# Kernel tuning notes

Measured on AMD Instinct MI355X. Metric: run time of the kernel, lower is better.

The kernel has to match this reference:

```python
import jax, jax.numpy as jnp
import numpy as np

NUM_HEADS = 8
NUM_Q = 64
RANK = 64
DIM = 768
LN_EPS = 1e-5


def setup_inputs() -> dict:
    key = jax.random.key(0)
    ks = jax.random.split(key, 8)
    b, n = 4, 1024
    x = jax.random.normal(ks[0], (b, NUM_Q, DIM), dtype=jnp.float32)
    context = jax.random.normal(ks[1], (b, n, DIM), dtype=jnp.float32)
    s = 0.02
    Wq = jax.random.normal(ks[2], (DIM, DIM), dtype=jnp.float32) * s
    Wk = jax.random.normal(ks[3], (DIM, DIM), dtype=jnp.float32) * s
    Wv1 = jax.random.normal(ks[4], (DIM, NUM_Q * RANK), dtype=jnp.float32) * s
    ln_g = jnp.ones((NUM_Q * RANK,), dtype=jnp.float32)
    ln_b = jnp.zeros((NUM_Q * RANK,), dtype=jnp.float32)
    Wc = jax.random.normal(ks[5], (NUM_Q, RANK, DIM), dtype=jnp.float32) * s
    Wout = jax.random.normal(ks[6], (DIM, DIM), dtype=jnp.float32) * s
    return {"x": x, "context": context, "Wq": Wq, "Wk": Wk, "Wv1": Wv1,
            "ln_g": ln_g, "ln_b": ln_b, "Wc": Wc, "Wout": Wout}


def reference(x, context, Wq, Wk, Wv1, ln_g, ln_b, Wc, Wout):
    b, nq, d = x.shape
    n = context.shape[1]
    h, dh = NUM_HEADS, d // NUM_HEADS

    q = x @ Wq                      # [b, nq, d]
    k = context @ Wk                # [b, n, d]

    # q-aware V: Linear -> LayerNorm(all_q_mid) -> grouped 1x1 conv (per-query rank->d)
    h1 = context @ Wv1              # [b, n, NUM_Q*RANK]
    mu = jnp.mean(h1, axis=-1, keepdims=True)
    var = jnp.var(h1, axis=-1, keepdims=True)
    h1 = (h1 - mu) * jax.lax.rsqrt(var + LN_EPS) * ln_g + ln_b
    vmid = h1.reshape(b, n, NUM_Q, RANK)
    v = jnp.einsum('bnqr,qrd->bqnd', vmid, Wc)   # [b, NUM_Q, n, d]
    # split heads: 'b q n (h dh) -> b h q n dh'
    v = v.reshape(b, NUM_Q, n, h, dh).transpose(0, 3, 1, 2, 4)

    qh = q.reshape(b, nq, h, dh).transpose(0, 2, 1, 3)   # [b,h,nq,dh]
    kh = k.reshape(b, n, h, dh).transpose(0, 2, 1, 3)    # [b,h,n,dh]
    scale = dh ** (-0.25)
    sim = jnp.einsum('bhid,bhjd->bhij', qh * scale, kh * scale)
    attn = jax.nn.softmax(sim, axis=-1)                  # [b,h,nq,n]
    out = jnp.einsum('bhij,bhijd->bhid', attn, v)        # per-query V
    out = out.transpose(0, 2, 1, 3).reshape(b, nq, d)
    return out @ Wout
```

## Files before the change

kernel.cpp:

```cpp
#include <hip/hip_runtime.h>
#include <math.h>

typedef unsigned short ushort_t;
typedef __bf16 bf16x8 __attribute__((ext_vector_type(8)));
typedef float f32x4 __attribute__((ext_vector_type(4)));

__device__ __forceinline__ ushort_t f2b_rne(float f) {
    union { float f; unsigned int u; } c;
    c.f = f;
    unsigned int u = c.u;
    u += 0x7FFFu + ((u >> 16) & 1u);
    return (ushort_t)(u >> 16);
}
__device__ __forceinline__ float b2f(ushort_t v) {
    union { unsigned int u; float f; } c;
    c.u = ((unsigned int)v) << 16;
    return c.f;
}

__device__ __forceinline__ void gl_lds16(const ushort_t* g, ushort_t* l) {
    __builtin_amdgcn_global_load_lds(
        (const __attribute__((address_space(1))) void*)g,
        (__attribute__((address_space(3))) void*)l, 16, 0, 0);
}

__global__ __launch_bounds__(256) void prep(
    const float* __restrict__ x, const float* __restrict__ context,
    const float* __restrict__ Wq, const float* __restrict__ Wk,
    const float* __restrict__ Wv1, const float* __restrict__ Wout,
    ushort_t* __restrict__ x_b, ushort_t* __restrict__ ctx_b,
    ushort_t* __restrict__ Wq_t, ushort_t* __restrict__ Wk_t,
    ushort_t* __restrict__ Wv1_t, ushort_t* __restrict__ Wout_t,
    int b, int n) {
    const int t = threadIdx.x;
    const int bid = blockIdx.x;
    const int nb_x = (b * 64 * 768 / 4) / 256;
    const int nb_c = (b * n * 768 / 4) / 256;

    if (bid < nb_x + nb_c) {
        const float* in = (bid < nb_x) ? x : context;
        ushort_t* outp = (bid < nb_x) ? x_b : ctx_b;
        const int i = ((bid < nb_x) ? bid : (bid - nb_x)) * 256 + t;
        float4 v = ((const float4*)in)[i];
        ushort_t o[4] = {f2b_rne(v.x), f2b_rne(v.y), f2b_rne(v.z), f2b_rne(v.w)};
        *(uint2*)&outp[(size_t)i * 4] = *(uint2*)o;
        return;
    }

    int u = bid - nb_x - nb_c;
    const float* in;
    ushort_t* outp;
    int R = 768, C = 768;
    if (u < 576)        { in = Wq;  outp = Wq_t; }
    else if (u < 1152)  { u -= 576;  in = Wk;  outp = Wk_t; }
    else if (u < 4224)  { u -= 1152; in = Wv1; outp = Wv1_t; C = 4096; }
    else                { u -= 4224; in = Wout; outp = Wout_t; }
    const int ct = C / 32;
    const int c0 = (u % ct) * 32, r0 = (u / ct) * 32;
    const int tx = t & 31, ty = t >> 5;

    __shared__ float tt[32][33];
#pragma unroll
    for (int i = 0; i < 4; i++)
        tt[ty + 8 * i][tx] = in[(size_t)(r0 + ty + 8 * i) * C + c0 + tx];
    __syncthreads();
#pragma unroll
    for (int i = 0; i < 4; i++)
        outp[(size_t)(c0 + ty + 8 * i) * R + r0 + tx] = f2b_rne(tt[tx][ty + 8 * i]);
}

__global__ __launch_bounds__(256) void gemm3(
    const ushort_t* __restrict__ x_b, const ushort_t* __restrict__ ctx_b,
    const ushort_t* __restrict__ Wq_t, const ushort_t* __restrict__ Wk_t,
    const ushort_t* __restrict__ Wv1_t,
    ushort_t* __restrict__ qb, ushort_t* __restrict__ kb,
    ushort_t* __restrict__ h1b, int b, int n) {
    const int bid = blockIdx.x;
    const int tq = (b * 64 / 128) * 6;
    const int tk = (b * n / 128) * 6;

    const ushort_t *A, *Bt;
    ushort_t* C;
    int N, row0, col0;
    if (bid < tq) {
        A = x_b; Bt = Wq_t; C = qb; N = 768;
        row0 = (bid / 6) * 128; col0 = (bid % 6) * 128;
    } else if (bid < tq + tk) {
        const int u = bid - tq;
        A = ctx_b; Bt = Wk_t; C = kb; N = 768;
        row0 = (u / 6) * 128; col0 = (u % 6) * 128;
    } else {
        const int u = bid - tq - tk;
        A = ctx_b; Bt = Wv1_t; C = h1b; N = 4096;
        row0 = (u / 32) * 128; col0 = (u % 32) * 128;
    }
    const int K = 768;

    __shared__ ushort_t As[128 * 32];
    __shared__ ushort_t Bs[128 * 32];

    const int t = threadIdx.x;
    const int lane = t & 63;
    const int wave = t >> 6;
    const int quad = lane >> 4;
    const int l15 = lane & 15;
    const int wm = (wave >> 1) * 64;
    const int wn = (wave & 1) * 64;

    const ushort_t* ga0 = A + (size_t)(row0 + (t >> 2)) * K + (t & 3) * 8;
    const ushort_t* ga1 = ga0 + (size_t)64 * K;
    const ushort_t* gb0 = Bt + (size_t)(col0 + (t >> 2)) * K + (t & 3) * 8;
    const ushort_t* gb1 = gb0 + (size_t)64 * K;

    ushort_t* lA0 = &As[wave * 512];
    ushort_t* lA1 = &As[2048 + wave * 512];
    ushort_t* lB0 = &Bs[wave * 512];
    ushort_t* lB1 = &Bs[2048 + wave * 512];

    f32x4 acc[4][4] = {};

    for (int k0 = 0; k0 < K; k0 += 32) {
        __syncthreads();
        gl_lds16(ga0 + k0, lA0);
        gl_lds16(ga1 + k0, lA1);
        gl_lds16(gb0 + k0, lB0);
        gl_lds16(gb1 + k0, lB1);
        __syncthreads();

        bf16x8 af[4], bfr[4];
#pragma unroll
        for (int i = 0; i < 4; i++)
            af[i] = *(const bf16x8*)&As[(wm + i * 16 + l15) * 32 + quad * 8];
#pragma unroll
        for (int j = 0; j < 4; j++)
            bfr[j] = *(const bf16x8*)&Bs[(wn + j * 16 + l15) * 32 + quad * 8];
#pragma unroll
        for (int i = 0; i < 4; i++)
#pragma unroll
            for (int j = 0; j < 4; j++)
                acc[i][j] = __builtin_amdgcn_mfma_f32_16x16x32_bf16(
                    af[i], bfr[j], acc[i][j], 0, 0, 0);
    }

#pragma unroll
    for (int i = 0; i < 4; i++)
#pragma unroll
        for (int j = 0; j < 4; j++)
#pragma unroll
            for (int r = 0; r < 4; r++) {
                const int row = row0 + wm + i * 16 + quad * 4 + r;
                const int col = col0 + wn + j * 16 + l15;
                C[(size_t)row * N + col] = f2b_rne(acc[i][j][r]);
            }
}

__global__ __launch_bounds__(256) void stats_scores(
    const ushort_t* __restrict__ h1b, const ushort_t* __restrict__ qb,
    const ushort_t* __restrict__ kb, float* __restrict__ mu,
    float* __restrict__ rstd, float* __restrict__ S, int b, int n) {
    __shared__ ushort_t sb[192 * 104];
    const int bid = blockIdx.x;
    const int t = threadIdx.x;

    if (bid < b * n) {
        float* red = (float*)sb;
        const ushort_t* p = h1b + (size_t)bid * 4096;
        float v[16];
#pragma unroll
        for (int g = 0; g < 2; g++) {
            bf16x8 xv = *(const bf16x8*)&p[(t + g * 256) * 8];
#pragma unroll
            for (int j = 0; j < 8; j++) v[g * 8 + j] = (float)xv[j];
        }
        float s = 0.f;
#pragma unroll
        for (int i = 0; i < 16; i++) s += v[i];
        red[t] = s;
        __syncthreads();
        for (int off = 128; off > 0; off >>= 1) {
            if (t < off) red[t] += red[t + off];
            __syncthreads();
        }
        const float m = red[0] * (1.0f / 4096.0f);
        __syncthreads();
        float s2 = 0.f;
#pragma unroll
        for (int i = 0; i < 16; i++) { const float d = v[i] - m; s2 += d * d; }
        red[t] = s2;
        __syncthreads();
        for (int off = 128; off > 0; off >>= 1) {
            if (t < off) red[t] += red[t + off];
            __syncthreads();
        }
        if (t == 0) {
            mu[bid] = m;
            rstd[bid] = rsqrtf(red[0] * (1.0f / 4096.0f) + 1e-5f);
        }
        return;
    }

    const int sid = bid - b * n;
    const int nt = n / 128;
    const int n0 = (sid % nt) * 128;
    const int bh = sid / nt;
    const int bb = bh >> 3, h = bh & 7;
    const int lane = t & 63, wave = t >> 6;
    const int quad = lane >> 4, l15 = lane & 15;
    const int wm = (wave >> 1) * 32;
    const int wn = (wave & 1) * 64;

    ushort_t* Qs = sb;
    ushort_t* Ks = sb + 64 * 104;

    for (int g = t; g < 768; g += 256) {
        const int r = g / 12, s = g - r * 12;
        *(bf16x8*)&Qs[r * 104 + s * 8] =
            *(const bf16x8*)&qb[(size_t)(bb * 64 + r) * 768 + h * 96 + s * 8];
    }
    for (int g = t; g < 1536; g += 256) {
        const int r = g / 12, s = g - r * 12;
        *(bf16x8*)&Ks[r * 104 + s * 8] =
            *(const bf16x8*)&kb[(size_t)(bb * n + n0 + r) * 768 + h * 96 + s * 8];
    }
    __syncthreads();

    f32x4 acc[2][4] = {};
#pragma unroll
    for (int ks = 0; ks < 3; ks++) {
        bf16x8 af[2], bfr[4];
#pragma unroll
        for (int i = 0; i < 2; i++)
            af[i] = *(const bf16x8*)&Qs[(wm + i * 16 + l15) * 104 + ks * 32 + quad * 8];
#pragma unroll
        for (int j = 0; j < 4; j++)
            bfr[j] = *(const bf16x8*)&Ks[(wn + j * 16 + l15) * 104 + ks * 32 + quad * 8];
#pragma unroll
        for (int i = 0; i < 2; i++)
#pragma unroll
            for (int j = 0; j < 4; j++)
                acc[i][j] = __builtin_amdgcn_mfma_f32_16x16x32_bf16(
                    af[i], bfr[j], acc[i][j], 0, 0, 0);
    }

    const float sc = 0.10206207261596575f;
    float* Sp = S + (size_t)bh * 64 * n;
#pragma unroll
    for (int i = 0; i < 2; i++)
#pragma unroll
        for (int j = 0; j < 4; j++)
#pragma unroll
            for (int r = 0; r < 4; r++) {
                const int row = wm + i * 16 + quad * 4 + r;
                const int col = n0 + wn + j * 16 + l15;
                Sp[(size_t)row * n + col] = acc[i][j][r] * sc;
            }
}

__global__ __launch_bounds__(256) void attn_pv(
    const float* __restrict__ S, const float* __restrict__ mu,
    const float* __restrict__ rstd, const ushort_t* __restrict__ h1b,
    float* __restrict__ Apart, int n, int nsp) {
    const int sp = blockIdx.x;
    const int bq = blockIdx.y;
    const int bb = bq >> 6, qi = bq & 63;
    const int k0 = sp * 128;
    const int tid = threadIdx.x;
    const int lane = tid & 63, w = tid >> 6;
    const int k = tid & 127, hg = tid >> 7;

    __shared__ float sS[2048];
    __shared__ float smu[128], srs[128];
    __shared__ float cw[16];
    __shared__ float sm[8], sl[8], swmu[8];

    const size_t Sbase = ((size_t)(bb * 512) + qi) * n + k0;
    for (int i = tid; i < 1024; i += 256) {
        const int h = i >> 7, kk = i & 127;
        sS[i] = S[Sbase + (size_t)h * 64 * n + kk];
    }
    if (tid < 128) {
        smu[tid] = mu[(size_t)bb * n + k0 + tid];
        srs[tid] = rstd[(size_t)bb * n + k0 + tid];
    }
    __syncthreads();

    float r4[4];
#pragma unroll
    for (int hh = 0; hh < 4; hh++) r4[hh] = sS[(hg * 4 + hh) * 128 + k];
#pragma unroll
    for (int off = 32; off > 0; off >>= 1)
#pragma unroll
        for (int hh = 0; hh < 4; hh++) r4[hh] = fmaxf(r4[hh], __shfl_down(r4[hh], off));
    if (lane == 0)
#pragma unroll
        for (int hh = 0; hh < 4; hh++) cw[w * 4 + hh] = r4[hh];
    __syncthreads();
    if (tid < 8) {
        const int g2 = tid >> 2, hh = tid & 3;
        sm[tid] = fmaxf(cw[(2 * g2) * 4 + hh], cw[(2 * g2 + 1) * 4 + hh]);
    }
    __syncthreads();

    float wm4[4];
#pragma unroll
    for (int hh = 0; hh < 4; hh++) {
        const int h = hg * 4 + hh;
        const float e = expf(sS[h * 128 + k] - sm[h]);
        const float wv = e * srs[k];
        sS[h * 128 + k] = wv;
        r4[hh] = e;
        wm4[hh] = wv * smu[k];
    }
#pragma unroll
    for (int off = 32; off > 0; off >>= 1)
#pragma unroll
        for (int hh = 0; hh < 4; hh++) r4[hh] += __shfl_down(r4[hh], off);
    if (lane == 0)
#pragma unroll
        for (int hh = 0; hh < 4; hh++) cw[w * 4 + hh] = r4[hh];
    __syncthreads();
    if (tid < 8) {
        const int g2 = tid >> 2, hh = tid & 3;
        sl[tid] = cw[(2 * g2) * 4 + hh] + cw[(2 * g2 + 1) * 4 + hh];
    }
    __syncthreads();
#pragma unroll
    for (int off = 32; off > 0; off >>= 1)
#pragma unroll
        for (int hh = 0; hh < 4; hh++) wm4[hh] += __shfl_down(wm4[hh], off);
    if (lane == 0)
#pragma unroll
        for (int hh = 0; hh < 4; hh++) cw[w * 4 + hh] = wm4[hh];
    __syncthreads();
    if (tid < 8) {
        const int g2 = tid >> 2, hh = tid & 3;
        swmu[tid] = cw[(2 * g2) * 4 + hh] + cw[(2 * g2 + 1) * 4 + hh];
    }

    const ushort_t* vp =
        h1b + ((size_t)bb * n + k0 + w * 32) * 4096 + qi * 64 + lane;
    float acc[8] = {};
    for (int o = 0; o < 32; o += 8) {
        float v[8];
#pragma unroll
        for (int j = 0; j < 8; j++) v[j] = b2f(vp[(size_t)(o + j) * 4096]);
#pragma unroll
        for (int h = 0; h < 8; h++) {
            const float4 wa = *(const float4*)&sS[h * 128 + w * 32 + o];
            const float4 wb = *(const float4*)&sS[h * 128 + w * 32 + o + 4];
            acc[h] += wa.x * v[0] + wa.y * v[1] + wa.z * v[2] + wa.w * v[3] +
                      wb.x * v[4] + wb.y * v[5] + wb.z * v[6] + wb.w * v[7];
        }
    }
    __syncthreads();
#pragma unroll
    for (int h = 0; h < 8; h++) sS[w * 512 + h * 64 + lane] = acc[h];
    __syncthreads();

    float* Ap = Apart + ((size_t)bq * nsp + sp) * 544;
#pragma unroll
    for (int s = 0; s < 2; s++) {
        const int o = tid + s * 256;
        Ap[o] = sS[o] + sS[512 + o] + sS[1024 + o] + sS[1536 + o];
    }
    if (tid < 8) {
        Ap[512 + tid] = sm[tid];
        Ap[520 + tid] = sl[tid];
        Ap[528 + tid] = swmu[tid];
    }
}

__global__ __launch_bounds__(256) void merge_wc(
    const float* __restrict__ Apart, const float* __restrict__ ln_g,
    const float* __restrict__ ln_b, const float* __restrict__ Wc,
    ushort_t* __restrict__ outp, int nsp) {
    const int bq = blockIdx.x;
    const int qi = bq & 63;
    const int tid = threadIdx.x;

    __shared__ float sA[512];
    __shared__ float sst[8 * 24];

    for (int i = tid; i < nsp * 24; i += 256) {
        const int sp = i / 24, j = i - sp * 24;
        sst[sp * 24 + j] = Apart[((size_t)bq * nsp + sp) * 544 + 512 + j];
    }
    __syncthreads();

#pragma unroll
    for (int s = 0; s < 2; s++) {
        const int o = tid + s * 256;
        const int h = o >> 6, rr = o & 63;
        float m = -1e30f;
        for (int sp = 0; sp < nsp; sp++) m = fmaxf(m, sst[sp * 24 + h]);
        float l = 0.f, wm = 0.f, v = 0.f;
        for (int sp = 0; sp < nsp; sp++) {
            const float scl = expf(sst[sp * 24 + h] - m);
            l += scl * sst[sp * 24 + 8 + h];
            wm += scl * sst[sp * 24 + 16 + h];
            v += scl * Apart[((size_t)bq * nsp + sp) * 544 + o];
        }
        const int c = qi * 64 + rr;
        sA[o] = ln_g[c] * ((v - wm) / l) + ln_b[c];
    }
    __syncthreads();

    for (int d = tid; d < 768; d += 256) {
        const int h = d / 96;
        const float* wp = Wc + (size_t)qi * 49152 + d;
        float a = 0.f;
#pragma unroll
        for (int r = 0; r < 64; r++) a += sA[h * 64 + r] * wp[(size_t)r * 768];
        outp[(size_t)bq * 768 + d] = f2b_rne(a);
    }
}

__global__ __launch_bounds__(256) void gemm_out(const ushort_t* __restrict__ A,
                                                const ushort_t* __restrict__ Bt,
                                                float* __restrict__ C,
                                                int M, int N, int K) {
    __shared__ ushort_t As[128 * 40];
    __shared__ ushort_t Bs[128 * 40];

    const int t = threadIdx.x;
    const int lane = t & 63;
    const int wave = t >> 6;
    const int quad = lane >> 4;
    const int l15 = lane & 15;
    const int wm = (wave >> 1) * 64;
    const int wn = (wave & 1) * 64;
    const int row0 = blockIdx.y * 128, col0 = blockIdx.x * 128;

    const int srow = t >> 2;
    const int sseg = t & 3;
    const ushort_t* ga0 = A + (size_t)(row0 + srow) * K + sseg * 8;
    const ushort_t* ga1 = A + (size_t)(row0 + srow + 64) * K + sseg * 8;
    const ushort_t* gb0 = Bt + (size_t)(col0 + srow) * K + sseg * 8;
    const ushort_t* gb1 = Bt + (size_t)(col0 + srow + 64) * K + sseg * 8;

    f32x4 acc[4][4] = {};

    bf16x8 ra0 = *(const bf16x8*)ga0;
    bf16x8 ra1 = *(const bf16x8*)ga1;
    bf16x8 rb0 = *(const bf16x8*)gb0;
    bf16x8 rb1 = *(const bf16x8*)gb1;

    for (int k0 = 0; k0 < K; k0 += 32) {
        __syncthreads();
        *(bf16x8*)&As[srow * 40 + sseg * 8] = ra0;
        *(bf16x8*)&As[(srow + 64) * 40 + sseg * 8] = ra1;
        *(bf16x8*)&Bs[srow * 40 + sseg * 8] = rb0;
        *(bf16x8*)&Bs[(srow + 64) * 40 + sseg * 8] = rb1;
        __syncthreads();
        if (k0 + 32 < K) {
            ra0 = *(const bf16x8*)(ga0 + k0 + 32);
            ra1 = *(const bf16x8*)(ga1 + k0 + 32);
            rb0 = *(const bf16x8*)(gb0 + k0 + 32);
            rb1 = *(const bf16x8*)(gb1 + k0 + 32);
        }
        bf16x8 af[4], bfr[4];
#pragma unroll
        for (int i = 0; i < 4; i++)
            af[i] = *(const bf16x8*)&As[(wm + i * 16 + l15) * 40 + quad * 8];
#pragma unroll
        for (int j = 0; j < 4; j++)
            bfr[j] = *(const bf16x8*)&Bs[(wn + j * 16 + l15) * 40 + quad * 8];
#pragma unroll
        for (int i = 0; i < 4; i++)
#pragma unroll
            for (int j = 0; j < 4; j++)
                acc[i][j] = __builtin_amdgcn_mfma_f32_16x16x32_bf16(
                    af[i], bfr[j], acc[i][j], 0, 0, 0);
    }

#pragma unroll
    for (int i = 0; i < 4; i++)
#pragma unroll
        for (int j = 0; j < 4; j++)
#pragma unroll
            for (int r = 0; r < 4; r++) {
                const int row = row0 + wm + i * 16 + quad * 4 + r;
                const int col = col0 + wn + j * 16 + l15;
                C[(size_t)row * N + col] = acc[i][j][r];
            }
}

extern "C" void kernel_launch(void* const* d_in, const int* in_sizes, int n_in,
                              void* d_out, int out_size, void* d_ws, size_t ws_size,
                              hipStream_t stream) {
    const float* x       = (const float*)d_in[0];
    const float* context = (const float*)d_in[1];
    const float* Wq      = (const float*)d_in[2];
    const float* Wk      = (const float*)d_in[3];
    const float* Wv1     = (const float*)d_in[4];
    const float* ln_g    = (const float*)d_in[5];
    const float* ln_b    = (const float*)d_in[6];
    const float* Wc      = (const float*)d_in[7];
    const float* Wout    = (const float*)d_in[8];
    float* out = (float*)d_out;

    const int b = in_sizes[0] / (64 * 768);
    const int n = in_sizes[1] / (b * 768);
    const int M  = b * 64;
    const int Mn = b * n;
    const int nsp = n / 128;

    float* ws = (float*)d_ws;
    size_t off = 0;
    float* S     = ws + off;  off += (size_t)b * 8 * 64 * n;
    float* Apart = ws + off;  off += (size_t)M * nsp * 544;
    float* muh   = ws + off;  off += (size_t)Mn;
    float* rstdh = ws + off;  off += (size_t)Mn;

    ushort_t* us = (ushort_t*)(ws + off);
    size_t uo = 0;
    ushort_t* x_b    = us + uo;  uo += (size_t)M * 768;
    ushort_t* ctx_b  = us + uo;  uo += (size_t)Mn * 768;
    ushort_t* qb     = us + uo;  uo += (size_t)M * 768;
    ushort_t* kb     = us + uo;  uo += (size_t)Mn * 768;
    ushort_t* h1b    = us + uo;  uo += (size_t)Mn * 4096;
    ushort_t* Wq_t   = us + uo;  uo += (size_t)768 * 768;
    ushort_t* Wk_t   = us + uo;  uo += (size_t)768 * 768;
    ushort_t* Wv1_t  = us + uo;  uo += (size_t)4096 * 768;
    ushort_t* Wout_t = us + uo;  uo += (size_t)768 * 768;
    ushort_t* outp_b = us + uo;  uo += (size_t)M * 768;

    const int nb_x = (M * 768 / 4) / 256;
    const int nb_c = (Mn * 768 / 4) / 256;
    prep<<<nb_x + nb_c + 576 * 3 + 3072, 256, 0, stream>>>(
        x, context, Wq, Wk, Wv1, Wout, x_b, ctx_b, Wq_t, Wk_t, Wv1_t, Wout_t, b, n);

    const int tq = (M / 128) * 6, tk = (Mn / 128) * 6, th = (Mn / 128) * 32;
    gemm3<<<tq + tk + th, 256, 0, stream>>>(x_b, ctx_b, Wq_t, Wk_t, Wv1_t,
                                            qb, kb, h1b, b, n);

    stats_scores<<<Mn + b * 8 * (n / 128), 256, 0, stream>>>(
        h1b, qb, kb, muh, rstdh, S, b, n);

    attn_pv<<<dim3(nsp, M), 256, 0, stream>>>(S, muh, rstdh, h1b, Apart, n, nsp);

    merge_wc<<<M, 256, 0, stream>>>(Apart, ln_g, ln_b, Wc, outp_b, nsp);

    gemm_out<<<dim3(6, M / 128), 256, 0, stream>>>(outp_b, Wout_t, out, M, 768, 768);
}
```

Before: 203.1 us.

## Fuse LayerNorm stats into h1 GEMM epilogue and fuse attention with merge

The h1 projection is now computed transposed (Wv1 rows by context tokens), and its GEMM epilogue accumulates per-token sum and sum-of-squares via atomics. This removes the separate LayerNorm statistics pass over h1. Attention, PV and the Wc merge become one kernel per query that runs full-length softmax and does the PV product with MFMA over contiguous transposed h1 rows, dropping the split-K partials buffer and the merge kernel. In exchange, variance comes from E[x^2]-mean^2, which is less precise, the atomics add contention, and each attention block now handles all n keys serially with lower grid parallelism.

```diff
diff --git a/kernel.cpp b/kernel.cpp
--- a/kernel.cpp
+++ b/kernel.cpp
@@ -31,6 +31,7 @@
     ushort_t* __restrict__ x_b, ushort_t* __restrict__ ctx_b,
     ushort_t* __restrict__ Wq_t, ushort_t* __restrict__ Wk_t,
     ushort_t* __restrict__ Wv1_t, ushort_t* __restrict__ Wout_t,
+    float* __restrict__ colzero,
     int b, int n) {
     const int t = threadIdx.x;
     const int bid = blockIdx.x;
@@ -48,6 +49,12 @@
     }
 
     int u = bid - nb_x - nb_c;
+    if (u >= 4800) {
+        const int idx = (u - 4800) * 256 + t;
+        ((float4*)colzero)[idx] = make_float4(0.f, 0.f, 0.f, 0.f);
+        return;
+    }
+
     const float* in;
     ushort_t* outp;
     int R = 768, C = 768;
@@ -74,14 +81,17 @@
     const ushort_t* __restrict__ Wq_t, const ushort_t* __restrict__ Wk_t,
     const ushort_t* __restrict__ Wv1_t,
     ushort_t* __restrict__ qb, ushort_t* __restrict__ kb,
-    ushort_t* __restrict__ h1b, int b, int n) {
+    ushort_t* __restrict__ h1t, float* __restrict__ colsum,
+    float* __restrict__ colsumsq, int b, int n) {
     const int bid = blockIdx.x;
     const int tq = (b * 64 / 128) * 6;
     const int tk = (b * n / 128) * 6;
+    const int Mn = b * n;
 
     const ushort_t *A, *Bt;
     ushort_t* C;
     int N, row0, col0;
+    bool is_h1 = false;
     if (bid < tq) {
         A = x_b; Bt = Wq_t; C = qb; N = 768;
         row0 = (bid / 6) * 128; col0 = (bid % 6) * 128;
@@ -91,8 +101,10 @@
         row0 = (u / 6) * 128; col0 = (u % 6) * 128;
     } else {
         const int u = bid - tq - tk;
-        A = ctx_b; Bt = Wv1_t; C = h1b; N = 4096;
-        row0 = (u / 32) * 128; col0 = (u % 32) * 128;
+        A = Wv1_t; Bt = ctx_b; C = h1t; N = Mn;
+        const int ct = Mn / 128;
+        row0 = (u / ct) * 128; col0 = (u % ct) * 128;
+        is_h1 = true;
     }
     const int K = 768;
 
@@ -152,65 +164,45 @@
                 const int col = col0 + wn + j * 16 + l15;
                 C[(size_t)row * N + col] = f2b_rne(acc[i][j][r]);
             }
-}
-
-__global__ __launch_bounds__(256) void stats_scores(
-    const ushort_t* __restrict__ h1b, const ushort_t* __restrict__ qb,
-    const ushort_t* __restrict__ kb, float* __restrict__ mu,
-    float* __restrict__ rstd, float* __restrict__ S, int b, int n) {
-    __shared__ ushort_t sb[192 * 104];
-    const int bid = blockIdx.x;
+
+    if (is_h1) {
+#pragma unroll
+        for (int j = 0; j < 4; j++) {
+            float vs = 0.f, vq = 0.f;
+#pragma unroll
+            for (int i = 0; i < 4; i++)
+#pragma unroll
+                for (int r = 0; r < 4; r++) {
+                    const float v = acc[i][j][r];
+                    vs += v;
+                    vq += v * v;
+                }
+            vs += __shfl_xor(vs, 16); vs += __shfl_xor(vs, 32);
+            vq += __shfl_xor(vq, 16); vq += __shfl_xor(vq, 32);
+            if (quad == 0) {
+                const int col = col0 + wn + j * 16 + l15;
+                atomicAdd(&colsum[col], vs);
+                atomicAdd(&colsumsq[col], vq);
+            }
+        }
+    }
+}
+
+__global__ __launch_bounds__(256) void scores_mfma(const ushort_t* __restrict__ qb,
+                                                   const ushort_t* __restrict__ kb,
+                                                   float* __restrict__ S, int n) {
+    const int nt = n / 128;
+    const int n0 = (blockIdx.x % nt) * 128;
+    const int bh = blockIdx.x / nt;
+    const int bb = bh >> 3, h = bh & 7;
     const int t = threadIdx.x;
-
-    if (bid < b * n) {
-        float* red = (float*)sb;
-        const ushort_t* p = h1b + (size_t)bid * 4096;
-        float v[16];
-#pragma unroll
-        for (int g = 0; g < 2; g++) {
-            bf16x8 xv = *(const bf16x8*)&p[(t + g * 256) * 8];
-#pragma unroll
-            for (int j = 0; j < 8; j++) v[g * 8 + j] = (float)xv[j];
-        }
-        float s = 0.f;
-#pragma unroll
-        for (int i = 0; i < 16; i++) s += v[i];
-        red[t] = s;
-        __syncthreads();
-        for (int off = 128; off > 0; off >>= 1) {
-            if (t < off) red[t] += red[t + off];
-            __syncthreads();
-        }
-        const float m = red[0] * (1.0f / 4096.0f);
-        __syncthreads();
-        float s2 = 0.f;
-#pragma unroll
-        for (int i = 0; i < 16; i++) { const float d = v[i] - m; s2 += d * d; }
-        red[t] = s2;
-        __syncthreads();
-        for (int off = 128; off > 0; off >>= 1) {
-            if (t < off) red[t] += red[t + off];
-            __syncthreads();
-        }
-        if (t == 0) {
-            mu[bid] = m;
-            rstd[bid] = rsqrtf(red[0] * (1.0f / 4096.0f) + 1e-5f);
-        }
-        return;
-    }
-
-    const int sid = bid - b * n;
-    const int nt = n / 128;
-    const int n0 = (sid % nt) * 128;
-    const int bh = sid / nt;
-    const int bb = bh >> 3, h = bh & 7;
     const int lane = t & 63, wave = t >> 6;
     const int quad = lane >> 4, l15 = lane & 15;
     const int wm = (wave >> 1) * 32;
     const int wn = (wave & 1) * 64;
 
-    ushort_t* Qs = sb;
-    ushort_t* Ks = sb + 64 * 104;
+    __shared__ ushort_t Qs[64 * 104];
+    __shared__ ushort_t Ks[128 * 104];
 
     for (int g = t; g < 768; g += 256) {
         const int r = g / 12, s = g - r * 12;
@@ -256,152 +248,99 @@
             }
 }
 
-__global__ __launch_bounds__(256) void attn_pv(
-    const float* __restrict__ S, const float* __restrict__ mu,
-    const float* __restrict__ rstd, const ushort_t* __restrict__ h1b,
-    float* __restrict__ Apart, int n, int nsp) {
-    const int sp = blockIdx.x;
-    const int bq = blockIdx.y;
+__global__ __launch_bounds__(256) void attn_fused(
+    const float* __restrict__ S, const float* __restrict__ colsum,
+    const float* __restrict__ colsumsq, const ushort_t* __restrict__ h1t,
+    const float* __restrict__ ln_g, const float* __restrict__ ln_b,
+    const float* __restrict__ Wc, ushort_t* __restrict__ outp,
+    int n, int Mn) {
+    const int bq = blockIdx.x;
     const int bb = bq >> 6, qi = bq & 63;
-    const int k0 = sp * 128;
     const int tid = threadIdx.x;
-    const int lane = tid & 63, w = tid >> 6;
-    const int k = tid & 127, hg = tid >> 7;
-
-    __shared__ float sS[2048];
-    __shared__ float smu[128], srs[128];
-    __shared__ float cw[16];
+    const int lane = tid & 63, wv = tid >> 6;
+    const int quad = lane >> 4, l15 = lane & 15;
+
+    __shared__ ushort_t sW[9 * 1032];
+    __shared__ ushort_t sH[64 * 264];
     __shared__ float sm[8], sl[8], swmu[8];
-
-    const size_t Sbase = ((size_t)(bb * 512) + qi) * n + k0;
-    for (int i = tid; i < 1024; i += 256) {
-        const int h = i >> 7, kk = i & 127;
-        sS[i] = S[Sbase + (size_t)h * 64 * n + kk];
-    }
-    if (tid < 128) {
-        smu[tid] = mu[(size_t)bb * n + k0 + tid];
-        srs[tid] = rstd[(size_t)bb * n + k0 + tid];
-    }
+    __shared__ float sA[512];
+
+    float* sMu = (float*)sH;
+    float* sRs = (float*)sH + 1024;
+
+    for (int i = tid; i < n; i += 256) {
+        const float cs = colsum[bb * n + i];
+        const float cq = colsumsq[bb * n + i];
+        const float m = cs * (1.0f / 4096.0f);
+        sMu[i] = m;
+        sRs[i] = rsqrtf(cq * (1.0f / 4096.0f) - m * m + 1e-5f);
+    }
+    for (int i = tid; i < 1032; i += 256) sW[8 * 1032 + i] = 0;
     __syncthreads();
 
-    float r4[4];
-#pragma unroll
-    for (int hh = 0; hh < 4; hh++) r4[hh] = sS[(hg * 4 + hh) * 128 + k];
-#pragma unroll
-    for (int off = 32; off > 0; off >>= 1)
-#pragma unroll
-        for (int hh = 0; hh < 4; hh++) r4[hh] = fmaxf(r4[hh], __shfl_down(r4[hh], off));
-    if (lane == 0)
-#pragma unroll
-        for (int hh = 0; hh < 4; hh++) cw[w * 4 + hh] = r4[hh];
+#pragma unroll
+    for (int s = 0; s < 2; s++) {
+        const int h = wv * 2 + s;
+        const float* Sp = S + ((size_t)(bb * 8 + h) * 64 + qi) * n;
+        float m = -1e30f;
+        for (int i = lane; i < n; i += 64) m = fmaxf(m, Sp[i]);
+#pragma unroll
+        for (int off = 32; off > 0; off >>= 1) m = fmaxf(m, __shfl_down(m, off));
+        m = __shfl(m, 0);
+        float l = 0.f, wm = 0.f;
+        for (int i = lane; i < n; i += 64) {
+            const float e = expf(Sp[i] - m);
+            const float w = e * sRs[i];
+            const ushort_t wb = f2b_rne(w);
+            sW[h * 1032 + i] = wb;
+            l += e;
+            wm += b2f(wb) * sMu[i];
+        }
+#pragma unroll
+        for (int off = 32; off > 0; off >>= 1) {
+            l += __shfl_down(l, off);
+            wm += __shfl_down(wm, off);
+        }
+        if (lane == 0) { sm[h] = m; sl[h] = l; swmu[h] = wm; }
+    }
+
+    const int mrow = (l15 < 8 ? l15 : 8) * 1032;
+    f32x4 acc[4] = {};
+    const int nch = n >> 8;
+    for (int ch = 0; ch < nch; ch++) {
+        __syncthreads();
+        for (int g = tid; g < 2048; g += 256) {
+            const int row = g >> 5, seg = g & 31;
+            *(bf16x8*)&sH[row * 264 + seg * 8] =
+                *(const bf16x8*)&h1t[(size_t)(qi * 64 + row) * Mn + bb * n +
+                                     ch * 256 + seg * 8];
+        }
+        __syncthreads();
+#pragma unroll
+        for (int ks = 0; ks < 8; ks++) {
+            const bf16x8 af = *(const bf16x8*)&sW[mrow + ch * 256 + ks * 32 + quad * 8];
+#pragma unroll
+            for (int j = 0; j < 4; j++) {
+                const bf16x8 bf = *(const bf16x8*)&sH[(j * 16 + l15) * 264 + ks * 32 + quad * 8];
+                acc[j] = __builtin_amdgcn_mfma_f32_16x16x32_bf16(af, bf, acc[j], 0, 0, 0);
+            }
+        }
+    }
     __syncthreads();
-    if (tid < 8) {
-        const int g2 = tid >> 2, hh = tid & 3;
-        sm[tid] = fmaxf(cw[(2 * g2) * 4 + hh], cw[(2 * g2 + 1) * 4 + hh]);
-    }
-    __syncthreads();
-
-    float wm4[4];
-#pragma unroll
-    for (int hh = 0; hh < 4; hh++) {
-        const int h = hg * 4 + hh;
-        const float e = expf(sS[h * 128 + k] - sm[h]);
-        const float wv = e * srs[k];
-        sS[h * 128 + k] = wv;
-        r4[hh] = e;
-        wm4[hh] = wv * smu[k];
-    }
-#pragma unroll
-    for (int off = 32; off > 0; off >>= 1)
-#pragma unroll
-        for (int hh = 0; hh < 4; hh++) r4[hh] += __shfl_down(r4[hh], off);
-    if (lane == 0)
-#pragma unroll
-        for (int hh = 0; hh < 4; hh++) cw[w * 4 + hh] = r4[hh];
-    __syncthreads();
-    if (tid < 8) {
-        const int g2 = tid >> 2, hh = tid & 3;
-        sl[tid] = cw[(2 * g2) * 4 + hh] + cw[(2 * g2 + 1) * 4 + hh];
-    }
-    __syncthreads();
-#pragma unroll
-    for (int off = 32; off > 0; off >>= 1)
-#pragma unroll
-        for (int hh = 0; hh < 4; hh++) wm4[hh] += __shfl_down(wm4[hh], off);
-    if (lane == 0)
-#pragma unroll
-        for (int hh = 0; hh < 4; hh++) cw[w * 4 + hh] = wm4[hh];
-    __syncthreads();
-    if (tid < 8) {
-        const int g2 = tid >> 2, hh = tid & 3;
-        swmu[tid] = cw[(2 * g2) * 4 + hh] + cw[(2 * g2 + 1) * 4 + hh];
-    }
-
-    const ushort_t* vp =
-        h1b + ((size_t)bb * n + k0 + w * 32) * 4096 + qi * 64 + lane;
-    float acc[8] = {};
-    for (int o = 0; o < 32; o += 8) {
-        float v[8];
-#pragma unroll
-        for (int j = 0; j < 8; j++) v[j] = b2f(vp[(size_t)(o + j) * 4096]);
-#pragma unroll
-        for (int h = 0; h < 8; h++) {
-            const float4 wa = *(const float4*)&sS[h * 128 + w * 32 + o];
-            const float4 wb = *(const float4*)&sS[h * 128 + w * 32 + o + 4];
-            acc[h] += wa.x * v[0] + wa.y * v[1] + wa.z * v[2] + wa.w * v[3] +
-                      wb.x * v[4] + wb.y * v[5] + wb.z * v[6] + wb.w * v[7];
-        }
-    }
-    __syncthreads();
-#pragma unroll
-    for (int h = 0; h < 8; h++) sS[w * 512 + h * 64 + lane] = acc[h];
-    __syncthreads();
-
-    float* Ap = Apart + ((size_t)bq * nsp + sp) * 544;
-#pragma unroll
-    for (int s = 0; s < 2; s++) {
-        const int o = tid + s * 256;
-        Ap[o] = sS[o] + sS[512 + o] + sS[1024 + o] + sS[1536 + o];
-    }
-    if (tid < 8) {
-        Ap[512 + tid] = sm[tid];
-        Ap[520 + tid] = sl[tid];
-        Ap[528 + tid] = swmu[tid];
-    }
-}
-
-__global__ __launch_bounds__(256) void merge_wc(
-    const float* __restrict__ Apart, const float* __restrict__ ln_g,
-    const float* __restrict__ ln_b, const float* __restrict__ Wc,
-    ushort_t* __restrict__ outp, int nsp) {
-    const int bq = blockIdx.x;
-    const int qi = bq & 63;
-    const int tid = threadIdx.x;
-
-    __shared__ float sA[512];
-    __shared__ float sst[8 * 24];
-
-    for (int i = tid; i < nsp * 24; i += 256) {
-        const int sp = i / 24, j = i - sp * 24;
-        sst[sp * 24 + j] = Apart[((size_t)bq * nsp + sp) * 544 + 512 + j];
-    }
-    __syncthreads();
-
-#pragma unroll
-    for (int s = 0; s < 2; s++) {
-        const int o = tid + s * 256;
-        const int h = o >> 6, rr = o & 63;
-        float m = -1e30f;
-        for (int sp = 0; sp < nsp; sp++) m = fmaxf(m, sst[sp * 24 + h]);
-        float l = 0.f, wm = 0.f, v = 0.f;
-        for (int sp = 0; sp < nsp; sp++) {
-            const float scl = expf(sst[sp * 24 + h] - m);
-            l += scl * sst[sp * 24 + 8 + h];
-            wm += scl * sst[sp * 24 + 16 + h];
-            v += scl * Apart[((size_t)bq * nsp + sp) * 544 + o];
-        }
-        const int c = qi * 64 + rr;
-        sA[o] = ln_g[c] * ((v - wm) / l) + ln_b[c];
+
+    if (wv == 0) {
+#pragma unroll
+        for (int j = 0; j < 4; j++)
+#pragma unroll
+            for (int r = 0; r < 4; r++) {
+                const int h = quad * 4 + r;
+                if (h < 8) {
+                    const int rr = j * 16 + l15;
+                    const int c = qi * 64 + rr;
+                    sA[h * 64 + rr] =
+                        ln_g[c] * ((acc[j][r] - swmu[h]) / sl[h]) + ln_b[c];
+                }
+            }
     }
     __syncthreads();
 
@@ -503,14 +442,12 @@
     const int n = in_sizes[1] / (b * 768);
     const int M  = b * 64;
     const int Mn = b * n;
-    const int nsp = n / 128;
 
     float* ws = (float*)d_ws;
     size_t off = 0;
-    float* S     = ws + off;  off += (size_t)b * 8 * 64 * n;
-    float* Apart = ws + off;  off += (size_t)M * nsp * 544;
-    float* muh   = ws + off;  off += (size_t)Mn;
-    float* rstdh = ws + off;  off += (size_t)Mn;
+    float* S       = ws + off;  off += (size_t)b * 8 * 64 * n;
+    float* colsum  = ws + off;  off += (size_t)Mn;
+    float* colsumsq= ws + off;  off += (size_t)Mn;
 
     ushort_t* us = (ushort_t*)(ws + off);
     size_t uo = 0;
@@ -518,7 +455,7 @@
     ushort_t* ctx_b  = us + uo;  uo += (size_t)Mn * 768;
     ushort_t* qb     = us + uo;  uo += (size_t)M * 768;
     ushort_t* kb     = us + uo;  uo += (size_t)Mn * 768;
-    ushort_t* h1b    = us + uo;  uo += (size_t)Mn * 4096;
+    ushort_t* h1t    = us + uo;  uo += (size_t)Mn * 4096;
     ushort_t* Wq_t   = us + uo;  uo += (size_t)768 * 768;
     ushort_t* Wk_t   = us + uo;  uo += (size_t)768 * 768;
     ushort_t* Wv1_t  = us + uo;  uo += (size_t)4096 * 768;
@@ -527,19 +464,19 @@
 
     const int nb_x = (M * 768 / 4) / 256;
     const int nb_c = (Mn * 768 / 4) / 256;
-    prep<<<nb_x + nb_c + 576 * 3 + 3072, 256, 0, stream>>>(
-        x, context, Wq, Wk, Wv1, Wout, x_b, ctx_b, Wq_t, Wk_t, Wv1_t, Wout_t, b, n);
-
-    const int tq = (M / 128) * 6, tk = (Mn / 128) * 6, th = (Mn / 128) * 32;
+    prep<<<nb_x + nb_c + 4800 + 8, 256, 0, stream>>>(
+        x, context, Wq, Wk, Wv1, Wout, x_b, ctx_b, Wq_t, Wk_t, Wv1_t, Wout_t,
+        colsum, b, n);
+
+    const int tq = (M / 128) * 6, tk = (Mn / 128) * 6;
+    const int th = (4096 / 128) * (Mn / 128);
     gemm3<<<tq + tk + th, 256, 0, stream>>>(x_b, ctx_b, Wq_t, Wk_t, Wv1_t,
-                                            qb, kb, h1b, b, n);
-
-    stats_scores<<<Mn + b * 8 * (n / 128), 256, 0, stream>>>(
-        h1b, qb, kb, muh, rstdh, S, b, n);
-
-    attn_pv<<<dim3(nsp, M), 256, 0, stream>>>(S, muh, rstdh, h1b, Apart, n, nsp);
-
-    merge_wc<<<M, 256, 0, stream>>>(Apart, ln_g, ln_b, Wc, outp_b, nsp);
+                                            qb, kb, h1t, colsum, colsumsq, b, n);
+
+    scores_mfma<<<b * 8 * (n / 128), 256, 0, stream>>>(qb, kb, S, n);
+
+    attn_fused<<<M, 256, 0, stream>>>(S, colsum, colsumsq, h1t, ln_g, ln_b,
+                                      Wc, outp_b, n, Mn);
 
     gemm_out<<<dim3(6, M / 128), 256, 0, stream>>>(outp_b, Wout_t, out, M, 768, 768);
 }
```

Result: slower. 212.4 us (+4.6%).
